# Optimization experiments

Measured on AMD Instinct MI355X. Metric: run time of the kernel, lower is better.

## Reference

```python
import jax, jax.numpy as jnp
from jax import lax
import numpy as np

H = 64   # hidden_dim
R = 32   # rank


def setup_inputs() -> dict:
    key = jax.random.key(0)
    ks = jax.random.split(key, 18)
    B, C, T = 64, 256, 512
    s = 0.1
    f32 = jnp.float32
    return {
        "x": jax.random.normal(ks[0], (B, C, T), f32),
        "y": jax.random.normal(ks[1], (B, C, 1), f32),
        # GRU layer 0 (input_size=1)
        "W_ih0": (jax.random.normal(ks[2], (3 * H, 1), f32) * s),
        "W_hh0": (jax.random.normal(ks[3], (3 * H, H), f32) * s),
        "b_ih0": (jax.random.normal(ks[4], (3 * H,), f32) * s),
        "b_hh0": (jax.random.normal(ks[5], (3 * H,), f32) * s),
        # GRU layer 1 (input_size=H)
        "W_ih1": (jax.random.normal(ks[6], (3 * H, H), f32) * s),
        "W_hh1": (jax.random.normal(ks[7], (3 * H, H), f32) * s),
        "b_ih1": (jax.random.normal(ks[8], (3 * H,), f32) * s),
        "b_hh1": (jax.random.normal(ks[9], (3 * H,), f32) * s),
        # heads
        "W_mean": (jax.random.normal(ks[10], (1, H), f32) * s),
        "b_mean": (jax.random.normal(ks[11], (1,), f32) * s),
        "W_d": (jax.random.normal(ks[12], (1, H), f32) * s),
        "b_d": (jax.random.normal(ks[13], (1,), f32) * s),
        "W_v": (jax.random.normal(ks[14], (R, H), f32) * s),
        "b_v": (jax.random.normal(ks[15], (R,), f32) * s),
    }


def _gru_cell(xin, h, Wih, Whh, bih, bhh):
    # PyTorch GRU cell. xin: [N, in], h: [N, H]
    gx = xin @ Wih.T + bih            # [N, 3H]
    gh = h @ Whh.T + bhh              # [N, 3H]
    r = jax.nn.sigmoid(gx[:, :H] + gh[:, :H])
    z = jax.nn.sigmoid(gx[:, H:2 * H] + gh[:, H:2 * H])
    n = jnp.tanh(gx[:, 2 * H:] + r * gh[:, 2 * H:])
    return (1.0 - z) * n + z * h


def reference(x, y, W_ih0, W_hh0, b_ih0, b_hh0, W_ih1, W_hh1, b_ih1, b_hh1,
              W_mean, b_mean, W_d, b_d, W_v, b_v):
    B, C, T = x.shape
    N = B * C
    # Original loops the GRU over channels; channels are independent sequences,
    # so batch them all: [T, N, 1]
    xs = x.reshape(N, T).T[:, :, None]

    def step(carry, xt):
        h0, h1 = carry
        h0 = _gru_cell(xt, h0, W_ih0, W_hh0, b_ih0, b_hh0)
        h1 = _gru_cell(h0, h1, W_ih1, W_hh1, b_ih1, b_hh1)
        return (h0, h1), None

    h0 = jnp.zeros((N, H), x.dtype)
    (_, hT), _ = lax.scan(step, (h0, h0), xs)   # hT: last output of top layer
    hT = hT.reshape(B, C, H)

    mu = hT @ W_mean.T + b_mean                 # [B, C, 1]
    v = hT @ W_v.T + b_v                        # [B, C, R]
    d = jnp.log1p(jnp.exp(hT @ W_d.T + b_d))[..., 0]   # softplus, [B, C]

    sigma = jnp.einsum('bcr,bkr->bck', v, v) + jnp.eye(C, dtype=x.dtype) * d[:, :, None]
    resid = y - mu                              # [B, C, 1]
    inv = jnp.linalg.inv(sigma)
    quad = jnp.einsum('bci,bck,bkj->b', resid, inv, resid)
    logdet = jnp.linalg.slogdet(sigma)[1]
    return jnp.mean(quad + logdet)
```

## Files before the change

### kernel.cpp

```cpp
#include <hip/hip_runtime.h>

typedef __attribute__((ext_vector_type(8))) _Float16 f16x8;
typedef __attribute__((ext_vector_type(4))) float f32x4;

namespace {

constexpr int H_ = 64;
constexpr int R_ = 32;
constexpr int B_ = 64;
constexpr int C_ = 256;
constexpr int T_ = 512;
constexpr int N_ = B_ * C_;

constexpr float NLOG2E  = -1.44269504088896f;
constexpr float N2LOG2E = -2.88539008177793f;

#define MFMA16(a, b, c) __builtin_amdgcn_mfma_f32_16x16x32_f16((a), (b), (c), 0, 0, 0)

__device__ __forceinline__ float sig_fold(float pre, float cb) {
    float t = __builtin_amdgcn_exp2f(__fmaf_rn(pre, NLOG2E, cb));
    return __builtin_amdgcn_rcpf(1.0f + t);
}
__device__ __forceinline__ float tanh_fast(float a) {
    float t = __builtin_amdgcn_exp2f(a * N2LOG2E);
    return __fmaf_rn(2.0f, __builtin_amdgcn_rcpf(1.0f + t), -1.0f);
}

__global__ void pack_weights_kernel(const float* __restrict__ Whh0,
                                    const float* __restrict__ Wih1,
                                    const float* __restrict__ Whh1,
                                    _Float16* __restrict__ packed)
{
    const int b = blockIdx.x;
    const int w = b / 18, f = b % 18;
    const int l = threadIdx.x;
    const int c = l & 15, g = l >> 4;
    const int hb = w * 16;
    const int kk = f & 1;
    const float* src = Whh0;
    int row = 0;
    switch (f >> 1) {
        case 0: src = Whh0; row = hb + c;        break;
        case 1: src = Whh0; row = 64 + hb + c;   break;
        case 2: src = Whh0; row = 128 + hb + c;  break;
        case 3: src = Wih1; row = hb + c;        break;
        case 4: src = Whh1; row = hb + c;        break;
        case 5: src = Wih1; row = 64 + hb + c;   break;
        case 6: src = Whh1; row = 64 + hb + c;   break;
        case 7: src = Wih1; row = 128 + hb + c;  break;
        case 8: src = Whh1; row = 128 + hb + c;  break;
    }
    _Float16* dst = packed + ((size_t)(w * 18 + f) * 512) + (size_t)l * 8;
    #pragma unroll
    for (int j = 0; j < 8; ++j) {
        int k = kk * 32 + g * 8 + j;
        dst[j] = (_Float16)src[row * 64 + k];
    }
}


#define PHASE(PP, DT, DOL0, DOL1)                                             \
  do {                                                                        \
    const _Float16* h0rd = &h0s[(PP) ^ 1][0][0];                              \
    f16x8 a00 = *(const f16x8*)(h0rd + c * 72 + g * 8);                       \
    f16x8 a01 = *(const f16x8*)(h0rd + c * 72 + 32 + g * 8);                  \
    if (DOL0) {                                                               \
      f32x4 accr = MFMA16(a01, B[1], MFMA16(a00, B[0], zv));                  \
      f32x4 accz = MFMA16(a01, B[3], MFMA16(a00, B[2], zv));                  \
      f32x4 accn = MFMA16(a01, B[5], MFMA16(a00, B[4], zv));                  \
      if (DOL1) {                                                             \
        const _Float16* h1rd = &h1s[(PP) ^ 1][0][0];                          \
        f16x8 ah0 = *(const f16x8*)(h1rd + c * 72 + g * 8);                   \
        f16x8 ah1 = *(const f16x8*)(h1rd + c * 72 + 32 + g * 8);              \
        f32x4 r1  = MFMA16(ah1, B[9],  MFMA16(ah0, B[8],                      \
                    MFMA16(a01, B[7],  MFMA16(a00, B[6],  zv))));             \
        f32x4 z1  = MFMA16(ah1, B[13], MFMA16(ah0, B[12],                     \
                    MFMA16(a01, B[11], MFMA16(a00, B[10], zv))));             \
        _Pragma("unroll")                                                     \
        for (int q = 0; q < 4; ++q) {                                         \
          int seq = g * 4 + q;                                                \
          float xv = xs_[DT][seq];                                            \
          float r = sig_fold(__fmaf_rn(xv, wr0, accr[q]), cb0r);              \
          float z = sig_fold(__fmaf_rn(xv, wz0, accz[q]), cb0z);              \
          float np = __fmaf_rn(r, accn[q] + b0nh, __fmaf_rn(xv, wn0, b0nx));  \
          float nn = tanh_fast(np);                                           \
          float hn = __fmaf_rn(z, h0st[q] - nn, nn);                          \
          h0st[q] = hn;                                                       \
          h0s[PP][seq][hid] = (_Float16)hn;                                   \
        }                                                                     \
        f32x4 xn1 = MFMA16(a01, B[15], MFMA16(a00, B[14], zv));               \
        f32x4 hn1 = MFMA16(ah1, B[17], MFMA16(ah0, B[16], zv));               \
        _Pragma("unroll")                                                     \
        for (int q = 0; q < 4; ++q) {                                         \
          int seq = g * 4 + q;                                                \
          float r = sig_fold(r1[q], cb1r);                                    \
          float z = sig_fold(z1[q], cb1z);                                    \
          float np = __fmaf_rn(r, hn1[q] + b1nh, xn1[q] + b1nx);              \
          float nn = tanh_fast(np);                                           \
          float hn = __fmaf_rn(z, h1st[q] - nn, nn);                          \
          h1st[q] = hn;                                                       \
          h1s[PP][seq][hid] = (_Float16)hn;                                   \
        }                                                                     \
      } else {                                                                \
        _Pragma("unroll")                                                     \
        for (int q = 0; q < 4; ++q) {                                         \
          int seq = g * 4 + q;                                                \
          float xv = xs_[DT][seq];                                            \
          float r = sig_fold(__fmaf_rn(xv, wr0, accr[q]), cb0r);              \
          float z = sig_fold(__fmaf_rn(xv, wz0, accz[q]), cb0z);              \
          float np = __fmaf_rn(r, accn[q] + b0nh, __fmaf_rn(xv, wn0, b0nx));  \
          float nn = tanh_fast(np);                                           \
          float hn = __fmaf_rn(z, h0st[q] - nn, nn);                          \
          h0st[q] = hn;                                                       \
          h0s[PP][seq][hid] = (_Float16)hn;                                   \
        }                                                                     \
      }                                                                       \
    } else {                                                                  \
      const _Float16* h1rd = &h1s[(PP) ^ 1][0][0];                            \
      f16x8 ah0 = *(const f16x8*)(h1rd + c * 72 + g * 8);                     \
      f16x8 ah1 = *(const f16x8*)(h1rd + c * 72 + 32 + g * 8);                \
      f32x4 r1  = MFMA16(ah1, B[9],  MFMA16(ah0, B[8],                        \
                  MFMA16(a01, B[7],  MFMA16(a00, B[6],  zv))));               \
      f32x4 z1  = MFMA16(ah1, B[13], MFMA16(ah0, B[12],                       \
                  MFMA16(a01, B[11], MFMA16(a00, B[10], zv))));               \
      f32x4 xn1 = MFMA16(a01, B[15], MFMA16(a00, B[14], zv));                 \
      f32x4 hn1 = MFMA16(ah1, B[17], MFMA16(ah0, B[16], zv));                 \
      _Pragma("unroll")                                                       \
      for (int q = 0; q < 4; ++q) {                                           \
        float r = sig_fold(r1[q], cb1r);                                      \
        float z = sig_fold(z1[q], cb1z);                                      \
        float np = __fmaf_rn(r, hn1[q] + b1nh, xn1[q] + b1nx);                \
        float nn = tanh_fast(np);                                             \
        float hn = __fmaf_rn(z, h1st[q] - nn, nn);                            \
        h1st[q] = hn;                                                         \
      }                                                                       \
    }                                                                         \
  } while (0)

__global__ __launch_bounds__(256, 3)
void gru_mfma_kernel(const float* __restrict__ x,
                     const _Float16* __restrict__ packedW,
                     const float* __restrict__ Wih0,
                     const float* __restrict__ bih0,
                     const float* __restrict__ bhh0,
                     const float* __restrict__ bih1,
                     const float* __restrict__ bhh1,
                     float* __restrict__ hT_out)
{
    __shared__ __align__(16) _Float16 h0s[2][16][72];
    __shared__ __align__(16) _Float16 h1s[2][16][72];
    __shared__ float xs_[32][17];

    const int tid = threadIdx.x;
    const int l = tid & 63;
    const int w = tid >> 6;
    const int c = l & 15, g = l >> 4;
    const int hb = w * 16;
    const int hid = hb + c;
    const int n0 = blockIdx.x * 16;

    f16x8 B[18];
    {
        const f16x8* bp = (const f16x8*)(packedW + (size_t)w * 18 * 512);
        #pragma unroll
        for (int f = 0; f < 18; ++f) B[f] = bp[f * 64 + l];
    }

    const float wr0 = Wih0[hid], wz0 = Wih0[64 + hid], wn0 = Wih0[128 + hid];
    const float cb0r = NLOG2E * (bhh0[hid] + bih0[hid]);
    const float cb0z = NLOG2E * (bhh0[64 + hid] + bih0[64 + hid]);
    const float b0nh = bhh0[128 + hid];
    const float b0nx = bih0[128 + hid];
    const float cb1r = NLOG2E * (bih1[hid] + bhh1[hid]);
    const float cb1z = NLOG2E * (bih1[64 + hid] + bhh1[64 + hid]);
    const float b1nx = bih1[128 + hid];
    const float b1nh = bhh1[128 + hid];

    for (int p = tid; p < 2 * 16 * 72; p += 256) {
        (&h0s[0][0][0])[p] = (_Float16)0.0f;
        (&h1s[0][0][0])[p] = (_Float16)0.0f;
    }
    float h0st[4] = {0.f, 0.f, 0.f, 0.f};
    float h1st[4] = {0.f, 0.f, 0.f, 0.f};

    auto stage_x = [&](int t0) {
        int ss = tid >> 4;
        int tb = tid & 15;
        xs_[tb][ss]      = x[(size_t)(n0 + ss) * T_ + t0 + tb];
        xs_[tb + 16][ss] = x[(size_t)(n0 + ss) * T_ + t0 + tb + 16];
    };

    const f32x4 zv = {0.f, 0.f, 0.f, 0.f};

    stage_x(0);
    __syncthreads();
    PHASE(0, 0, true, false);

    for (int p = 1; p < T_ - 1; p += 2) {
        __syncthreads();
        PHASE(1, p & 31, true, true);
        if (((p + 1) & 31) == 0) {
            __syncthreads();
            stage_x(p + 1);
        }
        __syncthreads();
        PHASE(0, (p + 1) & 31, true, true);
    }

    __syncthreads();
    PHASE(1, 31, true, true);

    __syncthreads();
    PHASE(0, 0, false, true);

    #pragma unroll
    for (int q = 0; q < 4; ++q) {
        int seq = g * 4 + q;
        hT_out[(size_t)(n0 + seq) * H_ + hid] = h1st[q];
    }
}

__global__ __launch_bounds__(256)
void heads_kernel(const float* __restrict__ hT,
                  const float* __restrict__ y,
                  const float* __restrict__ Wm, const float* __restrict__ bm,
                  const float* __restrict__ Wd, const float* __restrict__ bd,
                  const float* __restrict__ Wv, const float* __restrict__ bv,
                  float* __restrict__ v_out,
                  float* __restrict__ dd_out,
                  float* __restrict__ r_out)
{
    const int n = blockIdx.x * 256 + threadIdx.x;
    const float* h = hT + (size_t)n * H_;

    float hreg[H_];
    #pragma unroll
    for (int j = 0; j < H_; j += 4) {
        float4 q = *(const float4*)(h + j);
        hreg[j] = q.x; hreg[j + 1] = q.y; hreg[j + 2] = q.z; hreg[j + 3] = q.w;
    }
    float mu = bm[0], dv = bd[0];
    #pragma unroll
    for (int j = 0; j < H_; ++j) {
        mu = __fmaf_rn(Wm[j], hreg[j], mu);
        dv = __fmaf_rn(Wd[j], hreg[j], dv);
    }
    r_out[n]  = y[n] - mu;
    dd_out[n] = log1pf(__expf(dv));

    for (int k = 0; k < R_; ++k) {
        float acc = bv[k];
        #pragma unroll
        for (int j = 0; j < H_; ++j)
            acc = __fmaf_rn(Wv[k * H_ + j], hreg[j], acc);
        v_out[(size_t)n * R_ + k] = acc;
    }
}

__device__ __forceinline__ float block_reduce_sum256(float* red, int tid, float val)
{
    red[tid] = val;
    __syncthreads();
    for (int off = 128; off > 0; off >>= 1) {
        if (tid < off) red[tid] += red[tid + off];
        __syncthreads();
    }
    float r = red[0];
    __syncthreads();
    return r;
}

__global__ __launch_bounds__(256)
void woodbury_kernel(const float* __restrict__ v_in,
                     const float* __restrict__ dd_in,
                     const float* __restrict__ r_in,
                     float* __restrict__ batch_out)
{
    __shared__ float Vl[C_][R_ + 1];
    __shared__ float Vw[C_][R_ + 1];
    __shared__ float wi[C_];
    __shared__ float rl[C_];
    __shared__ float red[256];
    __shared__ float MA[R_][R_ + 1];
    __shared__ float uA[R_], yA[R_], wA[R_];

    const int tid = threadIdx.x;
    const int nb  = blockIdx.x * C_;

    for (int p = tid; p < C_ * R_; p += 256) {
        int cc = p >> 5, k = p & 31;
        Vl[cc][k] = v_in[(size_t)(nb + cc) * R_ + k];
    }
    float dval = dd_in[nb + tid];
    float winv = 1.0f / dval;
    float rv   = r_in[nb + tid];
    wi[tid] = winv;
    rl[tid] = rv;
    __syncthreads();

    for (int p = tid; p < C_ * R_; p += 256) {
        int cc = p >> 5, k = p & 31;
        Vw[cc][k] = Vl[cc][k] * wi[cc];
    }
    __syncthreads();

    float slogd = block_reduce_sum256(red, tid, __logf(dval));
    float rDr   = block_reduce_sum256(red, tid, rv * rv * winv);

    #pragma unroll
    for (int e = 0; e < 4; ++e) {
        int p = tid + e * 256;
        int i = p >> 5, j = p & 31;
        float acc = (i == j) ? 1.0f : 0.0f;
        for (int cc = 0; cc < C_; ++cc)
            acc = __fmaf_rn(Vw[cc][i], Vl[cc][j], acc);
        MA[i][j] = acc;
    }
    if (tid < R_) {
        float acc = 0.0f;
        for (int cc = 0; cc < C_; ++cc)
            acc = __fmaf_rn(Vw[cc][tid], rl[cc], acc);
        uA[tid] = acc;
    }
    __syncthreads();

    for (int k = 0; k < R_; ++k) {
        if (tid == 0) MA[k][k] = sqrtf(MA[k][k]);
        __syncthreads();
        if (tid > k && tid < R_) MA[tid][k] /= MA[k][k];
        __syncthreads();
        if (tid > k && tid < R_) {
            float ljk = MA[tid][k];
            for (int i2 = k + 1; i2 <= tid; ++i2)
                MA[tid][i2] -= ljk * MA[i2][k];
        }
        __syncthreads();
    }
    float ldm = block_reduce_sum256(red, tid,
                    (tid < R_) ? 2.0f * __logf(MA[tid][tid]) : 0.0f);

    if (tid == 0) {
        for (int k = 0; k < R_; ++k) {
            float sv = uA[k];
            for (int i2 = 0; i2 < k; ++i2) sv -= MA[k][i2] * yA[i2];
            yA[k] = sv / MA[k][k];
        }
        for (int k = R_ - 1; k >= 0; --k) {
            float sv = yA[k];
            for (int i2 = k + 1; i2 < R_; ++i2) sv -= MA[i2][k] * wA[i2];
            wA[k] = sv / MA[k][k];
        }
        float uw = 0.0f;
        for (int k = 0; k < R_; ++k) uw += wA[k] * uA[k];
        batch_out[blockIdx.x] = (rDr - uw) + slogd + ldm;
    }
}

__global__ void finalize_kernel(const float* __restrict__ bws, float* __restrict__ out)
{
    float v = bws[threadIdx.x];
    #pragma unroll
    for (int off = 32; off > 0; off >>= 1)
        v += __shfl_down(v, off, 64);
    if (threadIdx.x == 0) out[0] = v * (1.0f / 64.0f);
}

}

extern "C" void kernel_launch(void* const* d_in, const int* in_sizes, int n_in,
                              void* d_out, int out_size, void* d_ws, size_t ws_size,
                              hipStream_t stream)
{
    const float* x    = (const float*)d_in[0];
    const float* y    = (const float*)d_in[1];
    const float* Wih0 = (const float*)d_in[2];
    const float* Whh0 = (const float*)d_in[3];
    const float* bih0 = (const float*)d_in[4];
    const float* bhh0 = (const float*)d_in[5];
    const float* Wih1 = (const float*)d_in[6];
    const float* Whh1 = (const float*)d_in[7];
    const float* bih1 = (const float*)d_in[8];
    const float* bhh1 = (const float*)d_in[9];
    const float* Wm   = (const float*)d_in[10];
    const float* bm   = (const float*)d_in[11];
    const float* Wd   = (const float*)d_in[12];
    const float* bd   = (const float*)d_in[13];
    const float* Wv   = (const float*)d_in[14];
    const float* bv   = (const float*)d_in[15];

    char* ws = (char*)d_ws;
    float*    hT     = (float*)(ws + 0);
    float*    v_ws   = (float*)(ws + 4194304);
    float*    dd_ws  = (float*)(ws + 6291456);
    float*    r_ws   = (float*)(ws + 6356992);
    float*    b_ws   = (float*)(ws + 6422528);
    _Float16* packed = (_Float16*)(ws + 6423552);

    pack_weights_kernel<<<72, 64, 0, stream>>>(Whh0, Wih1, Whh1, packed);
    gru_mfma_kernel<<<N_ / 16, 256, 0, stream>>>(
        x, packed, Wih0, bih0, bhh0, bih1, bhh1, hT);
    heads_kernel<<<N_ / 256, 256, 0, stream>>>(
        hT, y, Wm, bm, Wd, bd, Wv, bv, v_ws, dd_ws, r_ws);
    woodbury_kernel<<<B_, 256, 0, stream>>>(v_ws, dd_ws, r_ws, b_ws);
    finalize_kernel<<<1, 64, 0, stream>>>(b_ws, (float*)d_out);
}
```

Before: 1.021 ms.

## Process two 16-sequence tiles per GRU block to interleave independent recurrences

Each GRU block now handles 32 sequences as two independent 16-sequence tiles, running the per-timestep phase twice between barriers with separate hidden-state registers. This gives each wave two independent MFMA and transcendental chains to interleave, hiding latency on the serial recurrence and halving barriers per sequence. The x values are also read as a vectorised float4 from a padded shared buffer. In exchange, register and LDS use per block grow and the occupancy hint drops from 3 to 2 blocks per CU, and the grid has half as many blocks.

```diff
diff --git a/kernel.cpp b/kernel.cpp
--- a/kernel.cpp
+++ b/kernel.cpp
@@ -59,9 +59,9 @@
 }
 
 
-#define PHASE(PP, DT, DOL0, DOL1)                                             \
+#define PHASE(PP, DT, SO, H0ST, H1ST, DOL0, DOL1)                             \
   do {                                                                        \
-    const _Float16* h0rd = &h0s[(PP) ^ 1][0][0];                              \
+    const _Float16* h0rd = &h0s[(PP) ^ 1][SO][0];                             \
     f16x8 a00 = *(const f16x8*)(h0rd + c * 72 + g * 8);                       \
     f16x8 a01 = *(const f16x8*)(h0rd + c * 72 + 32 + g * 8);                  \
     if (DOL0) {                                                               \
@@ -69,24 +69,25 @@
       f32x4 accz = MFMA16(a01, B[3], MFMA16(a00, B[2], zv));                  \
       f32x4 accn = MFMA16(a01, B[5], MFMA16(a00, B[4], zv));                  \
       if (DOL1) {                                                             \
-        const _Float16* h1rd = &h1s[(PP) ^ 1][0][0];                          \
+        const _Float16* h1rd = &h1s[(PP) ^ 1][SO][0];                         \
         f16x8 ah0 = *(const f16x8*)(h1rd + c * 72 + g * 8);                   \
         f16x8 ah1 = *(const f16x8*)(h1rd + c * 72 + 32 + g * 8);              \
         f32x4 r1  = MFMA16(ah1, B[9],  MFMA16(ah0, B[8],                      \
                     MFMA16(a01, B[7],  MFMA16(a00, B[6],  zv))));             \
         f32x4 z1  = MFMA16(ah1, B[13], MFMA16(ah0, B[12],                     \
                     MFMA16(a01, B[11], MFMA16(a00, B[10], zv))));             \
+        float4 xq = *(const float4*)(&xs_[DT][SO + g * 4]);                   \
         _Pragma("unroll")                                                     \
         for (int q = 0; q < 4; ++q) {                                         \
           int seq = g * 4 + q;                                                \
-          float xv = xs_[DT][seq];                                            \
+          float xv = ((const float*)&xq)[q];                                  \
           float r = sig_fold(__fmaf_rn(xv, wr0, accr[q]), cb0r);              \
           float z = sig_fold(__fmaf_rn(xv, wz0, accz[q]), cb0z);              \
           float np = __fmaf_rn(r, accn[q] + b0nh, __fmaf_rn(xv, wn0, b0nx));  \
           float nn = tanh_fast(np);                                           \
-          float hn = __fmaf_rn(z, h0st[q] - nn, nn);                          \
-          h0st[q] = hn;                                                       \
-          h0s[PP][seq][hid] = (_Float16)hn;                                   \
+          float hn = __fmaf_rn(z, H0ST[q] - nn, nn);                          \
+          H0ST[q] = hn;                                                       \
+          h0s[PP][SO + seq][hid] = (_Float16)hn;                              \
         }                                                                     \
         f32x4 xn1 = MFMA16(a01, B[15], MFMA16(a00, B[14], zv));               \
         f32x4 hn1 = MFMA16(ah1, B[17], MFMA16(ah0, B[16], zv));               \
@@ -97,26 +98,27 @@
           float z = sig_fold(z1[q], cb1z);                                    \
           float np = __fmaf_rn(r, hn1[q] + b1nh, xn1[q] + b1nx);              \
           float nn = tanh_fast(np);                                           \
-          float hn = __fmaf_rn(z, h1st[q] - nn, nn);                          \
-          h1st[q] = hn;                                                       \
-          h1s[PP][seq][hid] = (_Float16)hn;                                   \
+          float hn = __fmaf_rn(z, H1ST[q] - nn, nn);                          \
+          H1ST[q] = hn;                                                       \
+          h1s[PP][SO + seq][hid] = (_Float16)hn;                              \
         }                                                                     \
       } else {                                                                \
+        float4 xq = *(const float4*)(&xs_[DT][SO + g * 4]);                   \
         _Pragma("unroll")                                                     \
         for (int q = 0; q < 4; ++q) {                                         \
           int seq = g * 4 + q;                                                \
-          float xv = xs_[DT][seq];                                            \
+          float xv = ((const float*)&xq)[q];                                  \
           float r = sig_fold(__fmaf_rn(xv, wr0, accr[q]), cb0r);              \
           float z = sig_fold(__fmaf_rn(xv, wz0, accz[q]), cb0z);              \
           float np = __fmaf_rn(r, accn[q] + b0nh, __fmaf_rn(xv, wn0, b0nx));  \
           float nn = tanh_fast(np);                                           \
-          float hn = __fmaf_rn(z, h0st[q] - nn, nn);                          \
-          h0st[q] = hn;                                                       \
-          h0s[PP][seq][hid] = (_Float16)hn;                                   \
+          float hn = __fmaf_rn(z, H0ST[q] - nn, nn);                          \
+          H0ST[q] = hn;                                                       \
+          h0s[PP][SO + seq][hid] = (_Float16)hn;                              \
         }                                                                     \
       }                                                                       \
     } else {                                                                  \
-      const _Float16* h1rd = &h1s[(PP) ^ 1][0][0];                            \
+      const _Float16* h1rd = &h1s[(PP) ^ 1][SO][0];                           \
       f16x8 ah0 = *(const f16x8*)(h1rd + c * 72 + g * 8);                     \
       f16x8 ah1 = *(const f16x8*)(h1rd + c * 72 + 32 + g * 8);                \
       f32x4 r1  = MFMA16(ah1, B[9],  MFMA16(ah0, B[8],                        \
@@ -131,13 +133,13 @@
         float z = sig_fold(z1[q], cb1z);                                      \
         float np = __fmaf_rn(r, hn1[q] + b1nh, xn1[q] + b1nx);                \
         float nn = tanh_fast(np);                                             \
-        float hn = __fmaf_rn(z, h1st[q] - nn, nn);                            \
-        h1st[q] = hn;                                                         \
+        float hn = __fmaf_rn(z, H1ST[q] - nn, nn);                            \
+        H1ST[q] = hn;                                                         \
       }                                                                       \
     }                                                                         \
   } while (0)
 
-__global__ __launch_bounds__(256, 3)
+__global__ __launch_bounds__(256, 2)
 void gru_mfma_kernel(const float* __restrict__ x,
                      const _Float16* __restrict__ packedW,
                      const float* __restrict__ Wih0,
@@ -147,9 +149,9 @@
                      const float* __restrict__ bhh1,
                      float* __restrict__ hT_out)
 {
-    __shared__ __align__(16) _Float16 h0s[2][16][72];
-    __shared__ __align__(16) _Float16 h1s[2][16][72];
-    __shared__ float xs_[32][17];
+    __shared__ __align__(16) _Float16 h0s[2][32][72];
+    __shared__ __align__(16) _Float16 h1s[2][32][72];
+    __shared__ __align__(16) float xs_[32][36];
 
     const int tid = threadIdx.x;
     const int l = tid & 63;
@@ -157,7 +159,7 @@
     const int c = l & 15, g = l >> 4;
     const int hb = w * 16;
     const int hid = hb + c;
-    const int n0 = blockIdx.x * 16;
+    const int n0 = blockIdx.x * 32;
 
     f16x8 B[18];
     {
@@ -176,47 +178,58 @@
     const float b1nx = bih1[128 + hid];
     const float b1nh = bhh1[128 + hid];
 
-    for (int p = tid; p < 2 * 16 * 72; p += 256) {
+    for (int p = tid; p < 2 * 32 * 72; p += 256) {
         (&h0s[0][0][0])[p] = (_Float16)0.0f;
         (&h1s[0][0][0])[p] = (_Float16)0.0f;
     }
-    float h0st[4] = {0.f, 0.f, 0.f, 0.f};
-    float h1st[4] = {0.f, 0.f, 0.f, 0.f};
+    float h0A[4] = {0.f, 0.f, 0.f, 0.f};
+    float h1A[4] = {0.f, 0.f, 0.f, 0.f};
+    float h0B[4] = {0.f, 0.f, 0.f, 0.f};
+    float h1B[4] = {0.f, 0.f, 0.f, 0.f};
 
     auto stage_x = [&](int t0) {
-        int ss = tid >> 4;
-        int tb = tid & 15;
-        xs_[tb][ss]      = x[(size_t)(n0 + ss) * T_ + t0 + tb];
-        xs_[tb + 16][ss] = x[(size_t)(n0 + ss) * T_ + t0 + tb + 16];
+        int tb = tid & 31;
+        int s0 = tid >> 5;
+        #pragma unroll
+        for (int e = 0; e < 4; ++e) {
+            int ss = s0 + e * 8;
+            xs_[tb][ss] = x[(size_t)(n0 + ss) * T_ + t0 + tb];
+        }
     };
 
     const f32x4 zv = {0.f, 0.f, 0.f, 0.f};
 
     stage_x(0);
     __syncthreads();
-    PHASE(0, 0, true, false);
+    PHASE(0, 0, 0,  h0A, h1A, true, false);
+    PHASE(0, 0, 16, h0B, h1B, true, false);
 
     for (int p = 1; p < T_ - 1; p += 2) {
         __syncthreads();
-        PHASE(1, p & 31, true, true);
+        PHASE(1, p & 31, 0,  h0A, h1A, true, true);
+        PHASE(1, p & 31, 16, h0B, h1B, true, true);
         if (((p + 1) & 31) == 0) {
             __syncthreads();
             stage_x(p + 1);
         }
         __syncthreads();
-        PHASE(0, (p + 1) & 31, true, true);
-    }
-
-    __syncthreads();
-    PHASE(1, 31, true, true);
-
-    __syncthreads();
-    PHASE(0, 0, false, true);
+        PHASE(0, (p + 1) & 31, 0,  h0A, h1A, true, true);
+        PHASE(0, (p + 1) & 31, 16, h0B, h1B, true, true);
+    }
+
+    __syncthreads();
+    PHASE(1, 31, 0,  h0A, h1A, true, true);
+    PHASE(1, 31, 16, h0B, h1B, true, true);
+
+    __syncthreads();
+    PHASE(0, 0, 0,  h0A, h1A, false, true);
+    PHASE(0, 0, 16, h0B, h1B, false, true);
 
     #pragma unroll
     for (int q = 0; q < 4; ++q) {
         int seq = g * 4 + q;
-        hT_out[(size_t)(n0 + seq) * H_ + hid] = h1st[q];
+        hT_out[(size_t)(n0 + seq) * H_ + hid]      = h1A[q];
+        hT_out[(size_t)(n0 + 16 + seq) * H_ + hid] = h1B[q];
     }
 }
 
@@ -397,7 +410,7 @@
     _Float16* packed = (_Float16*)(ws + 6423552);
 
     pack_weights_kernel<<<72, 64, 0, stream>>>(Whh0, Wih1, Whh1, packed);
-    gru_mfma_kernel<<<N_ / 16, 256, 0, stream>>>(
+    gru_mfma_kernel<<<N_ / 32, 256, 0, stream>>>(
         x, packed, Wih0, bih0, bhh0, bih1, bhh1, hT);
     heads_kernel<<<N_ / 256, 256, 0, stream>>>(
         hT, y, Wm, bm, Wd, bd, Wv, bv, v_ws, dd_ws, r_ws);
```

Measured after the change: 1.085 ms. 1.06x slower.

## Move layer-0 recurrent weights to LDS, fuse gate math, raise occupancy

Applied to the files above, without the earlier changes.

Moves the six layer-0 W_hh fragments out of registers into shared memory and reloads them from LDS each step, so fewer VGPRs are held and launch bounds can go from 3 to 4 blocks per CU. The z-gate sigmoid and tanh are folded algebraically into one combine with a single reciprocal, which drops two rcp ops per element. The cost is extra LDS reads every timestep on a latency-bound recurrent loop, and the higher occupancy target could cause register spills.

```diff
diff --git a/kernel.cpp b/kernel.cpp
--- a/kernel.cpp
+++ b/kernel.cpp
@@ -17,13 +17,11 @@
 
 #define MFMA16(a, b, c) __builtin_amdgcn_mfma_f32_16x16x32_f16((a), (b), (c), 0, 0, 0)
 
-__device__ __forceinline__ float sig_fold(float pre, float cb) {
-    float t = __builtin_amdgcn_exp2f(__fmaf_rn(pre, NLOG2E, cb));
-    return __builtin_amdgcn_rcpf(1.0f + t);
-}
-__device__ __forceinline__ float tanh_fast(float a) {
-    float t = __builtin_amdgcn_exp2f(a * N2LOG2E);
-    return __fmaf_rn(2.0f, __builtin_amdgcn_rcpf(1.0f + t), -1.0f);
+__device__ __forceinline__ float gru_combine(float h, float t_n, float t_z) {
+    float vn  = 1.0f + t_n;
+    float num = __fmaf_rn(h, vn, (1.0f - t_n) * t_z);
+    float den = vn * (1.0f + t_z);
+    return num * __builtin_amdgcn_rcpf(den);
 }
 
 __global__ void pack_weights_kernel(const float* __restrict__ Whh0,
@@ -65,39 +63,54 @@
     f16x8 a00 = *(const f16x8*)(h0rd + c * 72 + g * 8);                       \
     f16x8 a01 = *(const f16x8*)(h0rd + c * 72 + 32 + g * 8);                  \
     if (DOL0) {                                                               \
-      f32x4 accr = MFMA16(a01, B[1], MFMA16(a00, B[0], zv));                  \
-      f32x4 accz = MFMA16(a01, B[3], MFMA16(a00, B[2], zv));                  \
-      f32x4 accn = MFMA16(a01, B[5], MFMA16(a00, B[4], zv));                  \
+      unsigned woff = wbase;                                                  \
+      asm volatile("" : "+v"(woff));                                          \
+      const _Float16* wp = wlds + woff;                                       \
+      f16x8 W0 = *(const f16x8*)(wp);                                         \
+      f16x8 W1 = *(const f16x8*)(wp + 512);                                   \
+      f16x8 W2 = *(const f16x8*)(wp + 1024);                                  \
+      f16x8 W3 = *(const f16x8*)(wp + 1536);                                  \
+      f16x8 W4 = *(const f16x8*)(wp + 2048);                                  \
+      f16x8 W5 = *(const f16x8*)(wp + 2560);                                  \
+      f32x4 accr = MFMA16(a01, W1, MFMA16(a00, W0, zv));                      \
+      f32x4 accz = MFMA16(a01, W3, MFMA16(a00, W2, zv));                      \
+      f32x4 accn = MFMA16(a01, W5, MFMA16(a00, W4, zv));                      \
       if (DOL1) {                                                             \
         const _Float16* h1rd = &h1s[(PP) ^ 1][0][0];                          \
         f16x8 ah0 = *(const f16x8*)(h1rd + c * 72 + g * 8);                   \
         f16x8 ah1 = *(const f16x8*)(h1rd + c * 72 + 32 + g * 8);              \
-        f32x4 r1  = MFMA16(ah1, B[9],  MFMA16(ah0, B[8],                      \
-                    MFMA16(a01, B[7],  MFMA16(a00, B[6],  zv))));             \
-        f32x4 z1  = MFMA16(ah1, B[13], MFMA16(ah0, B[12],                     \
-                    MFMA16(a01, B[11], MFMA16(a00, B[10], zv))));             \
+        f32x4 r1  = MFMA16(ah1, Br[3], MFMA16(ah0, Br[2],                     \
+                    MFMA16(a01, Br[1], MFMA16(a00, Br[0], zv))));             \
+        f32x4 z1  = MFMA16(ah1, Br[7], MFMA16(ah0, Br[6],                     \
+                    MFMA16(a01, Br[5], MFMA16(a00, Br[4], zv))));             \
         _Pragma("unroll")                                                     \
         for (int q = 0; q < 4; ++q) {                                         \
           int seq = g * 4 + q;                                                \
           float xv = xs_[DT][seq];                                            \
-          float r = sig_fold(__fmaf_rn(xv, wr0, accr[q]), cb0r);              \
-          float z = sig_fold(__fmaf_rn(xv, wz0, accz[q]), cb0z);              \
-          float np = __fmaf_rn(r, accn[q] + b0nh, __fmaf_rn(xv, wn0, b0nx));  \
-          float nn = tanh_fast(np);                                           \
-          float hn = __fmaf_rn(z, h0st[q] - nn, nn);                          \
+          float tr = __builtin_amdgcn_exp2f(                                  \
+              __fmaf_rn(__fmaf_rn(xv, wr0, accr[q]), NLOG2E, cb0r));          \
+          float r  = __builtin_amdgcn_rcpf(1.0f + tr);                        \
+          float tz = __builtin_amdgcn_exp2f(                                  \
+              __fmaf_rn(__fmaf_rn(xv, wz0, accz[q]), NLOG2E, cb0z));          \
+          float pn = __fmaf_rn(r, accn[q] + b0nh, __fmaf_rn(xv, wn0, b0nx));  \
+          float tn = __builtin_amdgcn_exp2f(pn * N2LOG2E);                    \
+          float hn = gru_combine(h0st[q], tn, tz);                            \
           h0st[q] = hn;                                                       \
           h0s[PP][seq][hid] = (_Float16)hn;                                   \
         }                                                                     \
-        f32x4 xn1 = MFMA16(a01, B[15], MFMA16(a00, B[14], zv));               \
-        f32x4 hn1 = MFMA16(ah1, B[17], MFMA16(ah0, B[16], zv));               \
+        f32x4 xn1 = MFMA16(a01, Br[9],  MFMA16(a00, Br[8],  zv));             \
+        f32x4 hn1 = MFMA16(ah1, Br[11], MFMA16(ah0, Br[10], zv));             \
         _Pragma("unroll")                                                     \
         for (int q = 0; q < 4; ++q) {                                         \
           int seq = g * 4 + q;                                                \
-          float r = sig_fold(r1[q], cb1r);                                    \
-          float z = sig_fold(z1[q], cb1z);                                    \
-          float np = __fmaf_rn(r, hn1[q] + b1nh, xn1[q] + b1nx);              \
-          float nn = tanh_fast(np);                                           \
-          float hn = __fmaf_rn(z, h1st[q] - nn, nn);                          \
+          float tr = __builtin_amdgcn_exp2f(                                  \
+              __fmaf_rn(r1[q], NLOG2E, cb1r));                                \
+          float r  = __builtin_amdgcn_rcpf(1.0f + tr);                        \
+          float tz = __builtin_amdgcn_exp2f(                                  \
+              __fmaf_rn(z1[q], NLOG2E, cb1z));                                \
+          float pn = __fmaf_rn(r, hn1[q] + b1nh, xn1[q] + b1nx);              \
+          float tn = __builtin_amdgcn_exp2f(pn * N2LOG2E);                    \
+          float hn = gru_combine(h1st[q], tn, tz);                            \
           h1st[q] = hn;                                                       \
           h1s[PP][seq][hid] = (_Float16)hn;                                   \
         }                                                                     \
@@ -106,11 +119,14 @@
         for (int q = 0; q < 4; ++q) {                                         \
           int seq = g * 4 + q;                                                \
           float xv = xs_[DT][seq];                                            \
-          float r = sig_fold(__fmaf_rn(xv, wr0, accr[q]), cb0r);              \
-          float z = sig_fold(__fmaf_rn(xv, wz0, accz[q]), cb0z);              \
-          float np = __fmaf_rn(r, accn[q] + b0nh, __fmaf_rn(xv, wn0, b0nx));  \
-          float nn = tanh_fast(np);                                           \
-          float hn = __fmaf_rn(z, h0st[q] - nn, nn);                          \
+          float tr = __builtin_amdgcn_exp2f(                                  \
+              __fmaf_rn(__fmaf_rn(xv, wr0, accr[q]), NLOG2E, cb0r));          \
+          float r  = __builtin_amdgcn_rcpf(1.0f + tr);                        \
+          float tz = __builtin_amdgcn_exp2f(                                  \
+              __fmaf_rn(__fmaf_rn(xv, wz0, accz[q]), NLOG2E, cb0z));          \
+          float pn = __fmaf_rn(r, accn[q] + b0nh, __fmaf_rn(xv, wn0, b0nx));  \
+          float tn = __builtin_amdgcn_exp2f(pn * N2LOG2E);                    \
+          float hn = gru_combine(h0st[q], tn, tz);                            \
           h0st[q] = hn;                                                       \
           h0s[PP][seq][hid] = (_Float16)hn;                                   \
         }                                                                     \
@@ -119,25 +135,26 @@
       const _Float16* h1rd = &h1s[(PP) ^ 1][0][0];                            \
       f16x8 ah0 = *(const f16x8*)(h1rd + c * 72 + g * 8);                     \
       f16x8 ah1 = *(const f16x8*)(h1rd + c * 72 + 32 + g * 8);                \
-      f32x4 r1  = MFMA16(ah1, B[9],  MFMA16(ah0, B[8],                        \
-                  MFMA16(a01, B[7],  MFMA16(a00, B[6],  zv))));               \
-      f32x4 z1  = MFMA16(ah1, B[13], MFMA16(ah0, B[12],                       \
-                  MFMA16(a01, B[11], MFMA16(a00, B[10], zv))));               \
-      f32x4 xn1 = MFMA16(a01, B[15], MFMA16(a00, B[14], zv));                 \
-      f32x4 hn1 = MFMA16(ah1, B[17], MFMA16(ah0, B[16], zv));                 \
+      f32x4 r1  = MFMA16(ah1, Br[3], MFMA16(ah0, Br[2],                       \
+                  MFMA16(a01, Br[1], MFMA16(a00, Br[0], zv))));               \
+      f32x4 z1  = MFMA16(ah1, Br[7], MFMA16(ah0, Br[6],                       \
+                  MFMA16(a01, Br[5], MFMA16(a00, Br[4], zv))));               \
+      f32x4 xn1 = MFMA16(a01, Br[9],  MFMA16(a00, Br[8],  zv));               \
+      f32x4 hn1 = MFMA16(ah1, Br[11], MFMA16(ah0, Br[10], zv));               \
       _Pragma("unroll")                                                       \
       for (int q = 0; q < 4; ++q) {                                           \
-        float r = sig_fold(r1[q], cb1r);                                      \
-        float z = sig_fold(z1[q], cb1z);                                      \
-        float np = __fmaf_rn(r, hn1[q] + b1nh, xn1[q] + b1nx);                \
-        float nn = tanh_fast(np);                                             \
-        float hn = __fmaf_rn(z, h1st[q] - nn, nn);                            \
+        float tr = __builtin_amdgcn_exp2f(__fmaf_rn(r1[q], NLOG2E, cb1r));    \
+        float r  = __builtin_amdgcn_rcpf(1.0f + tr);                          \
+        float tz = __builtin_amdgcn_exp2f(__fmaf_rn(z1[q], NLOG2E, cb1z));    \
+        float pn = __fmaf_rn(r, hn1[q] + b1nh, xn1[q] + b1nx);                \
+        float tn = __builtin_amdgcn_exp2f(pn * N2LOG2E);                      \
+        float hn = gru_combine(h1st[q], tn, tz);                              \
         h1st[q] = hn;                                                         \
       }                                                                       \
     }                                                                         \
   } while (0)
 
-__global__ __launch_bounds__(256, 3)
+__global__ __launch_bounds__(256, 4)
 void gru_mfma_kernel(const float* __restrict__ x,
                      const _Float16* __restrict__ packedW,
                      const float* __restrict__ Wih0,
@@ -150,6 +167,7 @@
     __shared__ __align__(16) _Float16 h0s[2][16][72];
     __shared__ __align__(16) _Float16 h1s[2][16][72];
     __shared__ float xs_[32][17];
+    __shared__ __align__(16) _Float16 wlds[4 * 6 * 512];
 
     const int tid = threadIdx.x;
     const int l = tid & 63;
@@ -158,12 +176,16 @@
     const int hb = w * 16;
     const int hid = hb + c;
     const int n0 = blockIdx.x * 16;
-
-    f16x8 B[18];
+    const unsigned wbase = (unsigned)((w * 6) * 512 + l * 8);
+
+    f16x8 Br[12];
     {
         const f16x8* bp = (const f16x8*)(packedW + (size_t)w * 18 * 512);
         #pragma unroll
-        for (int f = 0; f < 18; ++f) B[f] = bp[f * 64 + l];
+        for (int f = 0; f < 6; ++f)
+            *(f16x8*)&wlds[(w * 6 + f) * 512 + l * 8] = bp[f * 64 + l];
+        #pragma unroll
+        for (int f = 0; f < 12; ++f) Br[f] = bp[(6 + f) * 64 + l];
     }
 
     const float wr0 = Wih0[hid], wz0 = Wih0[64 + hid], wn0 = Wih0[128 + hid];
```

Measured after the change: 1.036 ms. No clear change (+1.5%).
